# Optimization experiments

Hardware: AMD Instinct MI355X
Metric: run time of the kernel (lower is better)

The kernel has to match this reference:

```python
import jax, jax.numpy as jnp
import numpy as np

RCR, RCA = 5.2, 3.5
ETA_R, ZETA, ETA_A = 16.0, 32.0, 8.0
SHF_R = 0.9 + 0.26875 * np.arange(16)            # 16 radial shifts
SHF_Z = (2.0 * np.arange(8) + 1.0) * np.pi / 16.0  # 8 angular shifts
SHF_A = 0.9 + 0.65 * np.arange(4)                # 4 angular-radial shifts
NUM_SPECIES = 4
_pm = np.zeros((NUM_SPECIES, NUM_SPECIES), np.int32)
_c = 0
for _s1 in range(NUM_SPECIES):
    for _s2 in range(_s1, NUM_SPECIES):
        _pm[_s1, _s2] = _pm[_s2, _s1] = _c
        _c += 1
PAIR_IDX = _pm  # unordered species pair -> 0..9 (torchani triu order)


def setup_inputs():
    key = jax.random.key(0)
    k1, k2 = jax.random.split(key)
    B, N = 512, 16
    species = jax.random.randint(k1, (B, N), 0, NUM_SPECIES)
    coordinates = jax.random.normal(k2, (B, N, 3), dtype=jnp.float32) * 2.0
    return {"species": species, "coordinates": coordinates}


def _aev(species, coordinates):
    B, N, _ = coordinates.shape
    dt = coordinates.dtype
    shfr = jnp.asarray(SHF_R, dt)
    shfz = jnp.asarray(SHF_Z, dt)
    shfa = jnp.asarray(SHF_A, dt)
    valid = species >= 0                                   # padding atoms have species = -1
    eye = jnp.eye(N, dtype=bool)
    pair_valid = valid[:, :, None] & valid[:, None, :] & ~eye          # [B,N,N]
    diff = coordinates[:, :, None, :] - coordinates[:, None, :, :]     # [B,N,N,3]
    d2 = jnp.sum(diff * diff, axis=-1)
    d = jnp.sqrt(jnp.where(pair_valid, d2, 1.0))                       # safe distances
    sp1h = jax.nn.one_hot(species, NUM_SPECIES, dtype=dt)              # [B,N,4]; zeros for padding

    # ---- radial AEV (cutoff Rcr) ----
    fcr = jnp.where(pair_valid & (d <= RCR), 0.5 * jnp.cos(jnp.pi * d / RCR) + 0.5, 0.0)
    rad = 0.25 * jnp.exp(-ETA_R * (d[..., None] - shfr) ** 2) * fcr[..., None]   # [B,N,N,16]
    radial_aev = jnp.einsum('bijr,bjs->bisr', rad, sp1h).reshape(B, N, NUM_SPECIES * 16)

    # ---- angular AEV (cutoff Rca) ----
    fca = jnp.where(pair_valid & (d <= RCA), 0.5 * jnp.cos(jnp.pi * d / RCA) + 0.5, 0.0)
    dot = jnp.einsum('bijx,bikx->bijk', diff, diff)                    # [B,N,N,N]
    cosang = jnp.clip(0.95 * dot / (d[:, :, :, None] * d[:, :, None, :]), -0.95, 0.95)
    ang = jnp.arccos(cosang)                                           # [B,N,N,N]
    f1 = ((1.0 + jnp.cos(ang[..., None] - shfz)) * 0.5) ** ZETA        # [B,N,N,N,8]
    davg = 0.5 * (d[:, :, :, None] + d[:, :, None, :])
    f2 = jnp.exp(-ETA_A * (davg[..., None] - shfa) ** 2)               # [B,N,N,N,4]
    tri = (fca[:, :, :, None] * fca[:, :, None, :]) * (~eye).astype(dt)[None, None]  # j != k
    # torchani subaev layout flattens (ShfA, ShfZ) -> 4*8 = 32
    ret = (tri[..., None, None] * f2[..., :, None] * f1[..., None, :]).reshape(B, N, N, N, 32)
    pair_oh = jax.nn.one_hot(jnp.asarray(PAIR_IDX), 10, dtype=dt)      # [4,4,10]
    w = jnp.einsum('bjs,bkt,stp->bjkp', sp1h, sp1h, pair_oh)           # [B,N,N,10]
    # torchani: 2*f1*f2*fc per UNORDERED pair; here ordered (j,k) double-counts -> net factor 1
    angular_aev = jnp.einsum('bijkf,bjkp->bipf', ret, w).reshape(B, N, 10 * 32)
    return jnp.concatenate([radial_aev, angular_aev], axis=-1)         # [B,N,384]


def reference(species, coordinates):
    return species, _aev(species, coordinates)
```

## Files before the change

### kernel.cpp

```cpp
#include <hip/hip_runtime.h>

#define NATOMS 16

__global__ __launch_bounds__(128, 8) void aev_kernel(const int* __restrict__ species,
                                                     const float* __restrict__ coords,
                                                     float* __restrict__ out,
                                                     int nmol) {
    const int t = threadIdx.x;
    const int w = t >> 6;
    const int l = t & 63;
    const int b = blockIdx.x >> 3;
    const int q = blockIdx.x & 7;
    const int i = q * 2 + w;

    __shared__ float sx[16], sy[16], sz[16];
    __shared__ int   ssp[16];
    __shared__ float sCZh[8], sSZh[8], sGa[4];
    __shared__ float dX[2][16], dY[2][16], dZ[2][16];
    __shared__ float sD[2][16], sRinv[2][16], sFca[2][16];
    __shared__ float rad[2][16][17];
    __shared__ int   hist[2][10], sBase[2][10], sCur[2][10];
    __shared__ float4 ebuf[2][120];

    if (t < 16) {
        int sp = species[b * 16 + t];
        ssp[t] = sp;
        sx[t] = coords[(b * 16 + t) * 3 + 0];
        sy[t] = coords[(b * 16 + t) * 3 + 1];
        sz[t] = coords[(b * 16 + t) * 3 + 2];
        if (q == 0) out[b * 16 + t] = (float)sp;
    }
    if (t < 8) {
        float ang = (2.f * (float)t + 1.f) * 0.19634954084936207f;
        sCZh[t] = 0.5f * __cosf(ang);
        sSZh[t] = 0.5f * __sinf(ang);
    }
    if (t < 4) {
        int tri = (t * (t - 1)) >> 1;
        sGa[t] = __expf(-6.76f * (float)tri);
    }
    if (l < 10) hist[w][l] = 0;
    __syncthreads();

    const int spi = ssp[i];

    if (l < 16) {
        int jj = l;
        int spj = ssp[jj];
        float dx = sx[i] - sx[jj];
        float dy = sy[i] - sy[jj];
        float dz = sz[i] - sz[jj];
        bool pv = (jj != i) && (spi >= 0) && (spj >= 0);
        float d2 = dx * dx + dy * dy + dz * dz;
        float d = sqrtf(pv ? d2 : 1.0f);
        float rinv = 1.0f / d;
        float fca = (pv && d <= 3.5f) ? (0.5f * __cosf(d * 0.8975979010256552f) + 0.5f) : 0.0f;
        float fcr = (pv && d <= 5.2f) ? (0.5f * __cosf(d * 0.6041515809446141f) + 0.5f) : 0.0f;
        dX[w][jj] = dx; dY[w][jj] = dy; dZ[w][jj] = dz;
        sD[w][jj] = d; sRinv[w][jj] = rinv; sFca[w][jj] = fca;
        float fcr4 = 0.25f * fcr;
        #pragma unroll
        for (int r = 0; r < 16; ++r) {
            float e = d - (0.9f + 0.26875f * (float)r);
            rad[w][jj][r] = fcr4 * __expf(-16.0f * e * e);
        }
    }
    __syncthreads();

    int j1 = -1, k1 = -1, p1 = -1, j2 = -1, k2 = -1, p2 = -1;
    {
        int s = l;
        float sq = sqrtf((float)(961 - 8 * s));
        int j = (int)floorf((31.0f - sq) * 0.5f);
        j = j < 0 ? 0 : (j > 14 ? 14 : j);
        int off = (j * (31 - j)) >> 1;
        if (s < off) { --j; off = (j * (31 - j)) >> 1; }
        else { int off2 = ((j + 1) * (30 - j)) >> 1; if (s >= off2) { ++j; off = off2; } }
        int k = j + 1 + (s - off);
        if (sFca[w][j] > 0.f && sFca[w][k] > 0.f) {
            int s1 = ssp[j], s2 = ssp[k];
            int lo = s1 < s2 ? s1 : s2, hi = s1 < s2 ? s2 : s1;
            p1 = lo * 4 + hi - ((lo * (lo + 1)) >> 1);
            j1 = j; k1 = k;
            atomicAdd(&hist[w][p1], 1);
        }
    }
    if (l + 64 < 120) {
        int s = l + 64;
        float sq = sqrtf((float)(961 - 8 * s));
        int j = (int)floorf((31.0f - sq) * 0.5f);
        j = j < 0 ? 0 : (j > 14 ? 14 : j);
        int off = (j * (31 - j)) >> 1;
        if (s < off) { --j; off = (j * (31 - j)) >> 1; }
        else { int off2 = ((j + 1) * (30 - j)) >> 1; if (s >= off2) { ++j; off = off2; } }
        int k = j + 1 + (s - off);
        if (sFca[w][j] > 0.f && sFca[w][k] > 0.f) {
            int s1 = ssp[j], s2 = ssp[k];
            int lo = s1 < s2 ? s1 : s2, hi = s1 < s2 ? s2 : s1;
            p2 = lo * 4 + hi - ((lo * (lo + 1)) >> 1);
            j2 = j; k2 = k;
            atomicAdd(&hist[w][p2], 1);
        }
    }
    __syncthreads();

    if (l < 10) {
        int sum = 0;
        for (int qq = 0; qq < l; ++qq) sum += hist[w][qq];
        sBase[w][l] = sum;
        sCur[w][l] = sum;
    }
    __syncthreads();

    #pragma unroll
    for (int slot = 0; slot < 2; ++slot) {
        int jj = slot == 0 ? j1 : j2;
        int kk = slot == 0 ? k1 : k2;
        int pp = slot == 0 ? p1 : p2;
        if (jj >= 0) {
            float fj = sFca[w][jj], fk = sFca[w][kk];
            float dot = dX[w][jj] * dX[w][kk] + dY[w][jj] * dY[w][kk] + dZ[w][jj] * dZ[w][kk];
            float ca = 0.95f * dot * sRinv[w][jj] * sRinv[w][kk];
            ca = fminf(0.95f, fmaxf(-0.95f, ca));
            float sa = sqrtf(1.0f - ca * ca);
            float davg = 0.5f * (sD[w][jj] + sD[w][kk]);
            float e0 = davg - 0.9f;
            float t0 = 2.0f * fj * fk * __expf(-8.0f * e0 * e0);
            float r1 = __expf(10.4f * davg - 12.74f);
            int idx = atomicAdd(&sCur[w][pp], 1);
            ebuf[w][idx] = make_float4(ca, sa, t0, r1);
        }
    }
    __syncthreads();

    float* base_o = out + (size_t)nmol * 16 + (size_t)(b * 16 + i) * 384;
    {
        int f = l & 31;
        int z = f & 7;
        int a = f >> 3;
        float czh = sCZh[z];
        float szh = sSZh[z];
        float ga = sGa[a];
        int a1 = a & 1, a2 = a & 2;
        #pragma unroll
        for (int pp = 0; pp < 5; ++pp) {
            int p = pp * 2 + (l >> 5);
            int st = sBase[w][p];
            int n = hist[w][p];
            float acc = 0.0f;
            for (int e = 0; e < n; ++e) {
                float4 v = ebuf[w][st + e];
                float c1 = fmaf(czh, v.x, fmaf(szh, v.y, 0.5f));
                float c2 = c1 * c1;
                float c4 = c2 * c2;
                float c8 = c4 * c4;
                float c16 = c8 * c8;
                float c32 = c16 * c16;
                float tt = v.z;
                float rsq = v.w * v.w;
                tt = a1 ? tt * v.w : tt;
                tt = a2 ? tt * rsq : tt;
                acc = fmaf(tt, c32, acc);
            }
            base_o[64 + p * 32 + f] = acc * ga;
        }
    }

    {
        int s_ = l >> 4, r_ = l & 15;
        float rv = 0.0f;
        #pragma unroll
        for (int jj = 0; jj < 16; ++jj)
            rv += (ssp[jj] == s_) ? rad[w][jj][r_] : 0.0f;
        base_o[l] = rv;
    }
}

extern "C" void kernel_launch(void* const* d_in, const int* in_sizes, int n_in,
                              void* d_out, int out_size, void* d_ws, size_t ws_size,
                              hipStream_t stream) {
    const int*   species = (const int*)d_in[0];
    const float* coords  = (const float*)d_in[1];
    float*       out     = (float*)d_out;
    int nmol = in_sizes[0] / NATOMS;
    aev_kernel<<<nmol * 8, 128, 0, stream>>>(species, coords, out, nmol);
}
```

Baseline: 70.01 us.

## Use one-wave blocks per atom and spread radial terms across lanes

```diff
diff --git a/kernel.cpp b/kernel.cpp
--- a/kernel.cpp
+++ b/kernel.cpp
@@ -2,70 +2,65 @@
 
 #define NATOMS 16
 
-__global__ __launch_bounds__(128, 8) void aev_kernel(const int* __restrict__ species,
-                                                     const float* __restrict__ coords,
-                                                     float* __restrict__ out,
-                                                     int nmol) {
-    const int t = threadIdx.x;
-    const int w = t >> 6;
-    const int l = t & 63;
-    const int b = blockIdx.x >> 3;
-    const int q = blockIdx.x & 7;
-    const int i = q * 2 + w;
+__global__ __launch_bounds__(64, 8) void aev_kernel(const int* __restrict__ species,
+                                                    const float* __restrict__ coords,
+                                                    float* __restrict__ out,
+                                                    int nmol) {
+    const int l = threadIdx.x;
+    const int bid = blockIdx.x;
+    const int b = bid >> 4;
+    const int i = bid & 15;
 
-    __shared__ float sx[16], sy[16], sz[16];
+    __shared__ float scm[48];
     __shared__ int   ssp[16];
-    __shared__ float sCZh[8], sSZh[8], sGa[4];
-    __shared__ float dX[2][16], dY[2][16], dZ[2][16];
-    __shared__ float sD[2][16], sRinv[2][16], sFca[2][16];
-    __shared__ float rad[2][16][17];
-    __shared__ int   hist[2][10], sBase[2][10], sCur[2][10];
-    __shared__ float4 ebuf[2][120];
+    __shared__ float dX[16], dY[16], dZ[16], sD[16], sRinv[16], sFca[16], sFcr4[16];
+    __shared__ float rad[16][17];
+    __shared__ int   hist[10], sBase[10], sCur[10];
+    __shared__ float4 ebuf[105];
 
-    if (t < 16) {
-        int sp = species[b * 16 + t];
-        ssp[t] = sp;
-        sx[t] = coords[(b * 16 + t) * 3 + 0];
-        sy[t] = coords[(b * 16 + t) * 3 + 1];
-        sz[t] = coords[(b * 16 + t) * 3 + 2];
-        if (q == 0) out[b * 16 + t] = (float)sp;
+    if (l < 48) scm[l] = coords[b * 48 + l];
+    if (l < 16) {
+        int sp = species[b * 16 + l];
+        ssp[l] = sp;
+        if (i == 0) out[b * 16 + l] = (float)sp;
     }
-    if (t < 8) {
-        float ang = (2.f * (float)t + 1.f) * 0.19634954084936207f;
-        sCZh[t] = 0.5f * __cosf(ang);
-        sSZh[t] = 0.5f * __sinf(ang);
-    }
-    if (t < 4) {
-        int tri = (t * (t - 1)) >> 1;
-        sGa[t] = __expf(-6.76f * (float)tri);
-    }
-    if (l < 10) hist[w][l] = 0;
+    if (l < 10) hist[l] = 0;
+
+    const int f = l & 31;
+    const int z = f & 7, a = f >> 3;
+    const float ang = (2.0f * (float)z + 1.0f) * 0.19634954084936207f;
+    const float czh = 0.5f * __cosf(ang);
+    const float szh = 0.5f * __sinf(ang);
+    const float ga  = __expf(-3.38f * (float)(a * a - a));
     __syncthreads();
 
     const int spi = ssp[i];
+    const float xi = scm[3 * i], yi = scm[3 * i + 1], zi = scm[3 * i + 2];
 
     if (l < 16) {
-        int jj = l;
-        int spj = ssp[jj];
-        float dx = sx[i] - sx[jj];
-        float dy = sy[i] - sy[jj];
-        float dz = sz[i] - sz[jj];
-        bool pv = (jj != i) && (spi >= 0) && (spj >= 0);
+        const int jj = l;
+        float dx = xi - scm[3 * jj], dy = yi - scm[3 * jj + 1], dz = zi - scm[3 * jj + 2];
+        bool pv = (jj != i) && (spi >= 0) && (ssp[jj] >= 0);
         float d2 = dx * dx + dy * dy + dz * dz;
         float d = sqrtf(pv ? d2 : 1.0f);
         float rinv = 1.0f / d;
         float fca = (pv && d <= 3.5f) ? (0.5f * __cosf(d * 0.8975979010256552f) + 0.5f) : 0.0f;
         float fcr = (pv && d <= 5.2f) ? (0.5f * __cosf(d * 0.6041515809446141f) + 0.5f) : 0.0f;
-        dX[w][jj] = dx; dY[w][jj] = dy; dZ[w][jj] = dz;
-        sD[w][jj] = d; sRinv[w][jj] = rinv; sFca[w][jj] = fca;
-        float fcr4 = 0.25f * fcr;
+        dX[jj] = dx; dY[jj] = dy; dZ[jj] = dz;
+        sD[jj] = d; sRinv[jj] = rinv; sFca[jj] = fca; sFcr4[jj] = 0.25f * fcr;
+    }
+    __syncthreads();
+
+    {
+        const int jj = l & 15, rg = l >> 4;
+        float d = sD[jj], f4 = sFcr4[jj];
         #pragma unroll
-        for (int r = 0; r < 16; ++r) {
+        for (int rr = 0; rr < 4; ++rr) {
+            int r = rg * 4 + rr;
             float e = d - (0.9f + 0.26875f * (float)r);
-            rad[w][jj][r] = fcr4 * __expf(-16.0f * e * e);
+            rad[jj][r] = f4 * __expf(-16.0f * e * e);
         }
     }
-    __syncthreads();
 
     int j1 = -1, k1 = -1, p1 = -1, j2 = -1, k2 = -1, p2 = -1;
     {
@@ -77,15 +72,15 @@
         if (s < off) { --j; off = (j * (31 - j)) >> 1; }
         else { int off2 = ((j + 1) * (30 - j)) >> 1; if (s >= off2) { ++j; off = off2; } }
         int k = j + 1 + (s - off);
-        if (sFca[w][j] > 0.f && sFca[w][k] > 0.f) {
+        if (sFca[j] > 0.f && sFca[k] > 0.f) {
             int s1 = ssp[j], s2 = ssp[k];
             int lo = s1 < s2 ? s1 : s2, hi = s1 < s2 ? s2 : s1;
             p1 = lo * 4 + hi - ((lo * (lo + 1)) >> 1);
             j1 = j; k1 = k;
-            atomicAdd(&hist[w][p1], 1);
+            atomicAdd(&hist[p1], 1);
         }
     }
-    if (l + 64 < 120) {
+    if (l < 56) {
         int s = l + 64;
         float sq = sqrtf((float)(961 - 8 * s));
         int j = (int)floorf((31.0f - sq) * 0.5f);
@@ -94,21 +89,21 @@
         if (s < off) { --j; off = (j * (31 - j)) >> 1; }
         else { int off2 = ((j + 1) * (30 - j)) >> 1; if (s >= off2) { ++j; off = off2; } }
         int k = j + 1 + (s - off);
-        if (sFca[w][j] > 0.f && sFca[w][k] > 0.f) {
+        if (sFca[j] > 0.f && sFca[k] > 0.f) {
             int s1 = ssp[j], s2 = ssp[k];
             int lo = s1 < s2 ? s1 : s2, hi = s1 < s2 ? s2 : s1;
             p2 = lo * 4 + hi - ((lo * (lo + 1)) >> 1);
             j2 = j; k2 = k;
-            atomicAdd(&hist[w][p2], 1);
+            atomicAdd(&hist[p2], 1);
         }
     }
     __syncthreads();
 
     if (l < 10) {
         int sum = 0;
-        for (int qq = 0; qq < l; ++qq) sum += hist[w][qq];
-        sBase[w][l] = sum;
-        sCur[w][l] = sum;
+        for (int qq = 0; qq < l; ++qq) sum += hist[qq];
+        sBase[l] = sum;
+        sCur[l] = sum;
     }
     __syncthreads();
 
@@ -118,38 +113,33 @@
         int kk = slot == 0 ? k1 : k2;
         int pp = slot == 0 ? p1 : p2;
         if (jj >= 0) {
-            float fj = sFca[w][jj], fk = sFca[w][kk];
-            float dot = dX[w][jj] * dX[w][kk] + dY[w][jj] * dY[w][kk] + dZ[w][jj] * dZ[w][kk];
-            float ca = 0.95f * dot * sRinv[w][jj] * sRinv[w][kk];
+            float fj = sFca[jj], fk = sFca[kk];
+            float dot = dX[jj] * dX[kk] + dY[jj] * dY[kk] + dZ[jj] * dZ[kk];
+            float ca = 0.95f * dot * sRinv[jj] * sRinv[kk];
             ca = fminf(0.95f, fmaxf(-0.95f, ca));
             float sa = sqrtf(1.0f - ca * ca);
-            float davg = 0.5f * (sD[w][jj] + sD[w][kk]);
+            float davg = 0.5f * (sD[jj] + sD[kk]);
             float e0 = davg - 0.9f;
             float t0 = 2.0f * fj * fk * __expf(-8.0f * e0 * e0);
             float r1 = __expf(10.4f * davg - 12.74f);
-            int idx = atomicAdd(&sCur[w][pp], 1);
-            ebuf[w][idx] = make_float4(ca, sa, t0, r1);
+            int idx = atomicAdd(&sCur[pp], 1);
+            ebuf[idx] = make_float4(ca, sa, t0, r1);
         }
     }
     __syncthreads();
 
     float* base_o = out + (size_t)nmol * 16 + (size_t)(b * 16 + i) * 384;
     {
-        int f = l & 31;
-        int z = f & 7;
-        int a = f >> 3;
-        float czh = sCZh[z];
-        float szh = sSZh[z];
-        float ga = sGa[a];
-        int a1 = a & 1, a2 = a & 2;
+        const int half = l >> 5;
+        const bool a1 = (a & 1), a2 = (a & 2) != 0;
         #pragma unroll
         for (int pp = 0; pp < 5; ++pp) {
-            int p = pp * 2 + (l >> 5);
-            int st = sBase[w][p];
-            int n = hist[w][p];
+            int p = pp * 2 + half;
+            int st = sBase[p];
+            int n = hist[p];
             float acc = 0.0f;
             for (int e = 0; e < n; ++e) {
-                float4 v = ebuf[w][st + e];
+                float4 v = ebuf[st + e];
                 float c1 = fmaf(czh, v.x, fmaf(szh, v.y, 0.5f));
                 float c2 = c1 * c1;
                 float c4 = c2 * c2;
@@ -167,11 +157,11 @@
     }
 
     {
-        int s_ = l >> 4, r_ = l & 15;
+        const int s_ = l >> 4, r_ = l & 15;
         float rv = 0.0f;
         #pragma unroll
         for (int jj = 0; jj < 16; ++jj)
-            rv += (ssp[jj] == s_) ? rad[w][jj][r_] : 0.0f;
+            rv += (ssp[jj] == s_) ? rad[jj][r_] : 0.0f;
         base_o[l] = rv;
     }
 }
@@ -183,5 +173,5 @@
     const float* coords  = (const float*)d_in[1];
     float*       out     = (float*)d_out;
     int nmol = in_sizes[0] / NATOMS;
-    aev_kernel<<<nmol * 8, 128, 0, stream>>>(species, coords, out, nmol);
+    aev_kernel<<<nmol * 16, 64, 0, stream>>>(species, coords, out, nmol);
 }
```

After: 70.86 us. About the same (+1.2%).
